# Kernel tuning notes

Measured on AMD Instinct MI355X. Metric: run time of the kernel, lower is better.

The kernel has to match this reference:

```python
import jax, jax.numpy as jnp
import numpy as np

B, S, D, H = 2, 2048, 1024, 16
HD = D // H


def setup_inputs() -> dict:
    key = jax.random.key(0)
    ks = jax.random.split(key, 6)
    scale = D ** -0.5
    return {
        "x": jax.random.normal(ks[0], (B, S, D), dtype=jnp.float32),
        "attn_mask": jnp.ones((B, S), dtype=bool),
        "wq": jax.random.normal(ks[1], (D, D), dtype=jnp.float32) * scale,
        "wk": jax.random.normal(ks[2], (D, D), dtype=jnp.float32) * scale,
        "wv": jax.random.normal(ks[3], (D, D), dtype=jnp.float32) * scale,
        "wo": jax.random.normal(ks[4], (D, D), dtype=jnp.float32) * scale,
        "bo": jax.random.normal(ks[5], (D,), dtype=jnp.float32) * 0.01,
    }


def reference(x, attn_mask, wq, wk, wv, wo, bo):
    b, s, d = x.shape
    # torch Linear: y = x @ W.T
    q = (x @ wq.T).reshape(b, s, H, HD).transpose(0, 2, 1, 3)  # (b,h,s,hd)
    k = (x @ wk.T).reshape(b, s, H, HD).transpose(0, 2, 1, 3)
    v = (x @ wv.T).reshape(b, s, H, HD).transpose(0, 2, 1, 3)
    scores = jnp.einsum("bhqd,bhkd->bhqk", q, k) * (HD ** -0.5)
    causal = jnp.triu(jnp.ones((s, s), dtype=bool), k=1)  # True above diagonal
    mask = causal[None, None, :, :] | (~attn_mask)[:, None, None, :]
    mask_value = jnp.finfo(scores.dtype).min / 2
    scores = jnp.where(mask, mask_value, scores)
    att = jax.nn.softmax(scores, axis=-1)
    ctx = jnp.einsum("bhqk,bhkd->bhqd", att, v)
    ctx = ctx.transpose(0, 2, 1, 3).reshape(b, s, d)
    return ctx @ wo.T + bo
```

## Files before the change

kernel.cpp:

```cpp
#include <hip/hip_runtime.h>
#include <stdint.h>

#define SEQ   2048
#define DMODEL 1024
#define NHEAD 16
#define HDIM  64
#define MTOT  4096

typedef short s16x8 __attribute__((ext_vector_type(8)));
typedef float f32x4 __attribute__((ext_vector_type(4)));
typedef float f32x16 __attribute__((ext_vector_type(16)));
typedef unsigned u32x4 __attribute__((ext_vector_type(4)));

#define LOG2E 1.44269504088896340736f

#if __has_builtin(__builtin_amdgcn_exp2f)
#define EXP2(x) __builtin_amdgcn_exp2f(x)
#else
#define EXP2(x) exp2f(x)
#endif

__device__ __forceinline__ short f2bf(float f) {
  union { float f; unsigned u; } v; v.f = f;
  unsigned u = v.u + 0x7fff + ((v.u >> 16) & 1);
  return (short)(u >> 16);
}

__device__ __forceinline__ void async_cp16(const void* g, void* l) {
  __builtin_amdgcn_global_load_lds(
      (const __attribute__((address_space(1))) void*)g,
      (__attribute__((address_space(3))) void*)l, 16, 0, 0);
}

__device__ __forceinline__ f32x4 mfma16(s16x8 a, s16x8 b, f32x4 c) {
  return __builtin_amdgcn_mfma_f32_16x16x32_bf16(a, b, c, 0, 0, 0);
}
__device__ __forceinline__ f32x16 mfma32(s16x8 a, s16x8 b, f32x16 c) {
  return __builtin_amdgcn_mfma_f32_32x32x16_bf16(a, b, c, 0, 0, 0);
}

__global__ __launch_bounds__(256) void cast_kernel(
    const float* __restrict__ x,  const float* __restrict__ wq,
    const float* __restrict__ wk, const float* __restrict__ wv,
    const float* __restrict__ wo,
    short* __restrict__ xb,  short* __restrict__ wqb,
    short* __restrict__ wkb, short* __restrict__ wvb, short* __restrict__ wob) {
  int i = blockIdx.x * 256 + threadIdx.x;
  const float4* src; short* dst; int off;
  const int XN = 1 << 20, WN = 1 << 18;
  if (i < XN)            { src = (const float4*)x;  dst = xb;  off = i; }
  else if (i < XN + WN)  { src = (const float4*)wq; dst = wqb; off = i - XN; }
  else if (i < XN + 2*WN){ src = (const float4*)wk; dst = wkb; off = i - XN - WN; }
  else if (i < XN + 3*WN){ src = (const float4*)wv; dst = wvb; off = i - XN - 2*WN; }
  else                   { src = (const float4*)wo; dst = wob; off = i - XN - 3*WN; }
  float4 v = src[off];
  short4 o; o.x = f2bf(v.x); o.y = f2bf(v.y); o.z = f2bf(v.z); o.w = f2bf(v.w);
  *(short4*)(dst + off * 4) = o;
}

__global__ __launch_bounds__(512, 2) void qkv_gemm(
    const short* __restrict__ xb,  const short* __restrict__ wqb,
    const short* __restrict__ wkb, const short* __restrict__ wvb,
    short* __restrict__ Q, short* __restrict__ K, short* __restrict__ Vt) {
  __shared__ short SMEM[32768];
  short (*Abuf)[4096] = reinterpret_cast<short (*)[4096]>(SMEM);
  short (*Bbuf)[3][4096] = reinterpret_cast<short (*)[3][4096]>(SMEM + 8192);
  const int tid = threadIdx.x;
  const int w = tid >> 6, lane = tid & 63;
  const int c = lane & 15, g = lane >> 4;
  const int wm = w >> 2, wn = w & 3;
  const int n0 = blockIdx.x * 128, m0 = blockIdx.y * 128;
  const int srow = lane >> 2, schunk = lane & 3;

  f32x4 acc[3][4][2] = {};

#define QKV_STAGE(KT, BS)                                                      \
  {                                                                            \
    async_cp16(xb + (m0 + w * 16 + srow) * 1024 + (KT) * 32 + schunk * 8,      \
               &Abuf[BS][w * 512]);                                            \
    async_cp16(wqb + (n0 + w * 16 + srow) * 1024 + (KT) * 32 + schunk * 8,     \
               &Bbuf[BS][0][w * 512]);                                         \
    async_cp16(wkb + (n0 + w * 16 + srow) * 1024 + (KT) * 32 + schunk * 8,     \
               &Bbuf[BS][1][w * 512]);                                         \
    async_cp16(wvb + (n0 + w * 16 + srow) * 1024 + (KT) * 32 + schunk * 8,     \
               &Bbuf[BS][2][w * 512]);                                         \
  }

  QKV_STAGE(0, 0)
  for (int kt = 0; kt < 32; ++kt) {
    __syncthreads();
    if (kt + 1 < 32) { QKV_STAGE(kt + 1, (kt + 1) & 1) }
    const int cur = kt & 1;
    s16x8 a[4];
#pragma unroll
    for (int t = 0; t < 4; ++t)
      a[t] = *(const s16x8*)&Abuf[cur][(wm * 64 + t * 16 + c) * 32 + g * 8];
#pragma unroll
    for (int z = 0; z < 3; ++z) {
      s16x8 b[2];
#pragma unroll
      for (int u = 0; u < 2; ++u)
        b[u] = *(const s16x8*)&Bbuf[cur][z][(wn * 32 + u * 16 + c) * 32 + g * 8];
#pragma unroll
      for (int t = 0; t < 4; ++t)
#pragma unroll
        for (int u = 0; u < 2; ++u)
          acc[z][t][u] = mfma16(a[t], b[u], acc[z][t][u]);
    }
  }

  short* E = SMEM;
  const int b0 = m0 >> 11, sbase = m0 & 2047, hgb = n0 >> 6;

#pragma unroll
  for (int z = 0; z < 3; ++z) {
    __syncthreads();
    if (z == 2) {
#pragma unroll
      for (int t = 0; t < 4; ++t)
#pragma unroll
        for (int u = 0; u < 2; ++u) {
          int col = wn * 32 + u * 16 + c;
          int m = wm * 64 + t * 16 + g * 4;
          int phys = (m >> 3) ^ (col & 15);
          short4 o;
          o.x = f2bf(acc[z][t][u][0]); o.y = f2bf(acc[z][t][u][1]);
          o.z = f2bf(acc[z][t][u][2]); o.w = f2bf(acc[z][t][u][3]);
          *(short4*)&E[col * 128 + phys * 8 + (m & 7)] = o;
        }
      __syncthreads();
#pragma unroll
      for (int p = 0; p < 4; ++p) {
        int R = p * 32 + (tid >> 4);
        int j = tid & 15;
        int phys = j ^ (R & 15);
        s16x8 v = *(const s16x8*)&E[R * 128 + phys * 8];
        int hloc = R >> 6, hd = R & 63;
        *(s16x8*)&Vt[(((b0 * 16 + hgb + hloc) * 64 + hd) * 2048) + sbase + j * 8] = v;
      }
    } else {
      const float scale = (z == 0) ? 0.125f * LOG2E : 1.0f;
#pragma unroll
      for (int t = 0; t < 4; ++t)
#pragma unroll
        for (int u = 0; u < 2; ++u)
#pragma unroll
          for (int r = 0; r < 4; ++r) {
            int m = wm * 64 + t * 16 + g * 4 + r;
            int col = wn * 32 + u * 16 + c;
            int phys = (col >> 3) ^ ((m >> 2) & 15);
            E[m * 128 + phys * 8 + (col & 7)] = f2bf(acc[z][t][u][r] * scale);
          }
      __syncthreads();
      short* __restrict__ dst = (z == 0) ? Q : K;
#pragma unroll
      for (int p = 0; p < 4; ++p) {
        int R = p * 64 + (tid >> 3);
        int j = tid & 7;
        int m = R >> 1, hloc = R & 1;
        int phys = (hloc * 8 + j) ^ ((m >> 2) & 15);
        s16x8 v = *(const s16x8*)&E[m * 128 + phys * 8];
        *(s16x8*)&dst[(((b0 * 16 + hgb + hloc) * 2048) + sbase + m) * 64 + j * 8] = v;
      }
    }
  }
}

#define STAGE_K(KT, BS)                                                        \
  _Pragma("unroll") for (int j = 0; j < 4; ++j) {                              \
    int idx = w * 4 + j;                                                       \
    int ks = idx >> 3, p = idx & 7;                                            \
    async_cp16(Kg + ((KT) * 128 + p * 16 + srow) * 64 + ks * 32 + sw8,         \
               &Kbuf[BS][ks][p * 512]);                                        \
  }
#define STAGE_V(KT)                                                            \
  _Pragma("unroll") for (int j = 0; j < 4; ++j) {                              \
    int idx = w * 4 + j;                                                       \
    int ks2 = idx >> 2, p = idx & 3;                                           \
    async_cp16(Vg + (p * 16 + srow) * 2048 + (KT) * 128 + ks2 * 32 + sw8,      \
               &Vlds[ks2][p * 512]);                                           \
  }

__global__ __launch_bounds__(256, 3) void attn_kernel(
    const short* __restrict__ Q, const short* __restrict__ K,
    const short* __restrict__ Vt, short* __restrict__ ctx) {
  __shared__ short Kbuf[2][2][128 * 32];
  __shared__ short Vlds[4][64 * 32];
  __shared__ float Llds[4][32];

  const int tid = threadIdx.x;
  const int w = tid >> 6, lane = tid & 63;
  const int n31 = lane & 31, h = lane >> 5;
  int bx = blockIdx.x;
  if (blockIdx.y >= 16) bx = 15 - bx;
  const int bh = blockIdx.y;
  const int qbase = bx * 128 + w * 32;
  const short* __restrict__ Qg = Q + bh * (SEQ * HDIM);
  const short* __restrict__ Kg = K + bh * (SEQ * HDIM);
  const short* __restrict__ Vg = Vt + bh * (SEQ * HDIM);
  const int srow = lane >> 2, schunk = lane & 3;
  const int sw8 = (schunk ^ ((srow >> 1) & 3)) * 8;
  const int rsw = (n31 >> 1) & 3;

  s16x8 qf[4];
#pragma unroll
  for (int ch = 0; ch < 4; ++ch)
    qf[ch] = *(const s16x8*)&Qg[(qbase + n31) * 64 + ch * 16 + h * 8];

  float l_run = 0.f;
  f32x16 oacc[2] = {};

  STAGE_K(0, 0)
  for (int kt = 0; kt <= bx; ++kt) {
    __syncthreads();
    if (kt < bx) { STAGE_K(kt + 1, (kt + 1) & 1) }
    STAGE_V(kt)

    const bool diag = (kt == bx);
    const int mtmax = diag ? w : 3;
    const short (*Kc)[128 * 32] = Kbuf[kt & 1];

    unsigned pk[4][8];
#pragma unroll
    for (int mt = 0; mt < 4; ++mt) {
      if (mt > mtmax) break;
      f32x16 st = {};
#pragma unroll
      for (int ch = 0; ch < 4; ++ch) {
        s16x8 ka = *(const s16x8*)
            &Kc[ch >> 1][(mt * 32 + n31) * 32 + ((((ch & 1) * 2 + h) ^ rsw) * 8)];
        st = mfma32(ka, qf[ch], st);
      }
      if (diag && mt == w) {
#pragma unroll
        for (int reg = 0; reg < 16; ++reg) {
          int krow = (reg & 3) + 8 * (reg >> 2) + 4 * h;
          if (krow > n31) st[reg] = -1e30f;
        }
      }
#pragma unroll
      for (int i = 0; i < 8; ++i) {
        float p0 = EXP2(st[2 * i]);
        float p1 = EXP2(st[2 * i + 1]);
        unsigned t0 = __float_as_uint(p0) & 0xffff0000u;
        unsigned t1 = __float_as_uint(p1) & 0xffff0000u;
        l_run += __uint_as_float(t0);
        l_run += __uint_as_float(t1);
        pk[mt][i] = (t0 >> 16) | t1;
      }
    }

    __syncthreads();

#pragma unroll
    for (int mt = 0; mt < 4; ++mt) {
      if (mt > mtmax) break;
#pragma unroll
      for (int kb2 = 0; kb2 < 2; ++kb2) {
        const int kb = mt * 2 + kb2;
        const unsigned q0 = pk[mt][kb2 * 4 + 0], q1 = pk[mt][kb2 * 4 + 1];
        const unsigned q2 = pk[mt][kb2 * 4 + 2], q3 = pk[mt][kb2 * 4 + 3];
        const unsigned x0 = __shfl_xor(q0, 32), x1 = __shfl_xor(q1, 32);
        const unsigned x2 = __shfl_xor(q2, 32), x3 = __shfl_xor(q3, 32);
        u32x4 av;
        av.x = h ? x2 : q0;
        av.y = h ? x3 : q1;
        av.z = h ? q2 : x0;
        av.w = h ? q3 : x1;
        s16x8 pa = __builtin_bit_cast(s16x8, av);
#pragma unroll
        for (int u = 0; u < 2; ++u) {
          s16x8 vf = *(const s16x8*)
              &Vlds[kb >> 1][(u * 32 + n31) * 32 + ((((kb & 1) * 2 + h) ^ rsw) * 8)];
          oacc[u] = mfma32(pa, vf, oacc[u]);
        }
      }
    }
  }

  float lf = l_run + __shfl_xor(l_run, 32);
  if (h == 0) Llds[w][n31] = lf;
  float inv[4][4];
#pragma unroll
  for (int gi = 0; gi < 4; ++gi) {
    float4 lv = *(const float4*)&Llds[w][gi * 8 + 4 * h];
    inv[gi][0] = 1.0f / lv.x; inv[gi][1] = 1.0f / lv.y;
    inv[gi][2] = 1.0f / lv.z; inv[gi][3] = 1.0f / lv.w;
  }

  const int b = bh >> 4, hh = bh & 15;
#pragma unroll
  for (int u = 0; u < 2; ++u)
#pragma unroll
    for (int gi = 0; gi < 4; ++gi)
#pragma unroll
      for (int ri = 0; ri < 4; ++ri) {
        int q = qbase + 8 * gi + 4 * h + ri;
        int hd = u * 32 + n31;
        ctx[(b * 2048 + q) * 1024 + hh * 64 + hd] =
            f2bf(oacc[u][gi * 4 + ri] * inv[gi][ri]);
      }
}

__global__ __launch_bounds__(256) void out_gemm(
    const short* __restrict__ ctx, const short* __restrict__ wob,
    const float* __restrict__ bo, float* __restrict__ out) {
  __shared__ short Abuf[2][128 * 32];
  __shared__ short Bbuf[2][64 * 32];
  const int tid = threadIdx.x;
  const int w = tid >> 6, lane = tid & 63;
  const int c = lane & 15, g = lane >> 4;
  const int wm = w >> 1, wn = w & 1;
  const int n0 = blockIdx.x * 64, m0 = blockIdx.y * 128;
  const int srow = lane >> 2, schunk = lane & 3;

  f32x4 acc[4][2] = {};

#define OUT_STAGE(KT, BS)                                                      \
  {                                                                            \
    _Pragma("unroll") for (int j = 0; j < 2; ++j) {                            \
      int p = w * 2 + j;                                                       \
      async_cp16(ctx + (m0 + p * 16 + srow) * 1024 + (KT) * 32 + schunk * 8,   \
                 &Abuf[BS][p * 512]);                                          \
    }                                                                          \
    async_cp16(wob + (n0 + w * 16 + srow) * 1024 + (KT) * 32 + schunk * 8,     \
               &Bbuf[BS][w * 512]);                                            \
  }

  OUT_STAGE(0, 0)
  for (int kt = 0; kt < 32; ++kt) {
    __syncthreads();
    if (kt + 1 < 32) { OUT_STAGE(kt + 1, (kt + 1) & 1) }
    const int cur = kt & 1;
    s16x8 a[4], b[2];
#pragma unroll
    for (int t = 0; t < 4; ++t)
      a[t] = *(const s16x8*)&Abuf[cur][(wm * 64 + t * 16 + c) * 32 + g * 8];
#pragma unroll
    for (int u = 0; u < 2; ++u)
      b[u] = *(const s16x8*)&Bbuf[cur][(wn * 32 + u * 16 + c) * 32 + g * 8];
#pragma unroll
    for (int t = 0; t < 4; ++t)
#pragma unroll
      for (int u = 0; u < 2; ++u)
        acc[t][u] = mfma16(a[t], b[u], acc[t][u]);
  }

#pragma unroll
  for (int t = 0; t < 4; ++t)
#pragma unroll
    for (int u = 0; u < 2; ++u) {
      int col = n0 + wn * 32 + u * 16 + c;
      float bias = bo[col];
#pragma unroll
      for (int r = 0; r < 4; ++r) {
        int m = m0 + wm * 64 + t * 16 + g * 4 + r;
        out[m * 1024 + col] = acc[t][u][r] + bias;
      }
    }
}

extern "C" void kernel_launch(void* const* d_in, const int* in_sizes, int n_in,
                              void* d_out, int out_size, void* d_ws, size_t ws_size,
                              hipStream_t stream) {
  const float* x  = (const float*)d_in[0];
  const float* wq = (const float*)d_in[2];
  const float* wk = (const float*)d_in[3];
  const float* wv = (const float*)d_in[4];
  const float* wo = (const float*)d_in[5];
  const float* bo = (const float*)d_in[6];

  char* ws = (char*)d_ws;
  short* xb  = (short*)(ws);
  short* wqb = (short*)(ws + (size_t)( 8 << 20));
  short* wkb = (short*)(ws + (size_t)(10 << 20));
  short* wvb = (short*)(ws + (size_t)(12 << 20));
  short* wob = (short*)(ws + (size_t)(14 << 20));
  short* Qb  = (short*)(ws + (size_t)(16 << 20));
  short* Kb  = (short*)(ws + (size_t)(24 << 20));
  short* Vtb = (short*)(ws + (size_t)(32 << 20));
  short* ctx = (short*)(ws + (size_t)(40 << 20));
  float* out = (float*)d_out;

  cast_kernel<<<dim3(8192), dim3(256), 0, stream>>>(x, wq, wk, wv, wo,
                                                    xb, wqb, wkb, wvb, wob);
  qkv_gemm<<<dim3(8, 32), dim3(512), 0, stream>>>(xb, wqb, wkb, wvb,
                                                  Qb, Kb, Vtb);
  attn_kernel<<<dim3(16, 32), dim3(256), 0, stream>>>(Qb, Kb, Vtb, ctx);
  out_gemm<<<dim3(16, 32), dim3(256), 0, stream>>>(ctx, wob, bo, out);
}
```

Before: 183.6 us.

## Use 32x32 MFMA with swizzled LDS in GEMMs and double attention q-tile per wave

Both projection GEMMs move from 16x16x32 to 32x32x16 bf16 MFMA and load their LDS tiles with an XOR swizzle, cutting LDS bank conflicts and the fragment loads issued per MFMA. The attention kernel now gives each wave 64 query rows (two 32-row sub-tiles) and each block 256 rows, so every K/V tile in LDS is reused by twice as many queries and the grid is halved. The cost is higher register pressure in attention (occupancy hint lowered from 3 to 2) and fewer blocks to balance the causal triangle.

Measured after the change: 232.4 us. 1.27x slower.

```diff
diff --git a/kernel.cpp b/kernel.cpp
--- a/kernel.cpp
+++ b/kernel.cpp
@@ -32,9 +32,6 @@
       (__attribute__((address_space(3))) void*)l, 16, 0, 0);
 }
 
-__device__ __forceinline__ f32x4 mfma16(s16x8 a, s16x8 b, f32x4 c) {
-  return __builtin_amdgcn_mfma_f32_16x16x32_bf16(a, b, c, 0, 0, 0);
-}
 __device__ __forceinline__ f32x16 mfma32(s16x8 a, s16x8 b, f32x16 c) {
   return __builtin_amdgcn_mfma_f32_32x32x16_bf16(a, b, c, 0, 0, 0);
 }
@@ -67,22 +64,24 @@
   short (*Bbuf)[3][4096] = reinterpret_cast<short (*)[3][4096]>(SMEM + 8192);
   const int tid = threadIdx.x;
   const int w = tid >> 6, lane = tid & 63;
-  const int c = lane & 15, g = lane >> 4;
+  const int n31 = lane & 31, hb = lane >> 5;
   const int wm = w >> 2, wn = w & 3;
   const int n0 = blockIdx.x * 128, m0 = blockIdx.y * 128;
   const int srow = lane >> 2, schunk = lane & 3;
-
-  f32x4 acc[3][4][2] = {};
+  const int sw8 = (schunk ^ ((srow >> 1) & 3)) * 8;
+  const int rsw = (n31 >> 1) & 3;
+
+  f32x16 acc[3][2] = {};
 
 #define QKV_STAGE(KT, BS)                                                      \
   {                                                                            \
-    async_cp16(xb + (m0 + w * 16 + srow) * 1024 + (KT) * 32 + schunk * 8,      \
+    async_cp16(xb + (m0 + w * 16 + srow) * 1024 + (KT) * 32 + sw8,             \
                &Abuf[BS][w * 512]);                                            \
-    async_cp16(wqb + (n0 + w * 16 + srow) * 1024 + (KT) * 32 + schunk * 8,     \
+    async_cp16(wqb + (n0 + w * 16 + srow) * 1024 + (KT) * 32 + sw8,            \
                &Bbuf[BS][0][w * 512]);                                         \
-    async_cp16(wkb + (n0 + w * 16 + srow) * 1024 + (KT) * 32 + schunk * 8,     \
+    async_cp16(wkb + (n0 + w * 16 + srow) * 1024 + (KT) * 32 + sw8,            \
                &Bbuf[BS][1][w * 512]);                                         \
-    async_cp16(wvb + (n0 + w * 16 + srow) * 1024 + (KT) * 32 + schunk * 8,     \
+    async_cp16(wvb + (n0 + w * 16 + srow) * 1024 + (KT) * 32 + sw8,            \
                &Bbuf[BS][2][w * 512]);                                         \
   }
 
@@ -91,21 +90,23 @@
     __syncthreads();
     if (kt + 1 < 32) { QKV_STAGE(kt + 1, (kt + 1) & 1) }
     const int cur = kt & 1;
-    s16x8 a[4];
-#pragma unroll
-    for (int t = 0; t < 4; ++t)
-      a[t] = *(const s16x8*)&Abuf[cur][(wm * 64 + t * 16 + c) * 32 + g * 8];
+    s16x8 a[2][2];
+#pragma unroll
+    for (int mt = 0; mt < 2; ++mt)
+#pragma unroll
+      for (int ks = 0; ks < 2; ++ks)
+        a[mt][ks] = *(const s16x8*)
+            &Abuf[cur][(wm * 64 + mt * 32 + n31) * 32 + (((ks * 2 + hb) ^ rsw) * 8)];
 #pragma unroll
     for (int z = 0; z < 3; ++z) {
-      s16x8 b[2];
-#pragma unroll
-      for (int u = 0; u < 2; ++u)
-        b[u] = *(const s16x8*)&Bbuf[cur][z][(wn * 32 + u * 16 + c) * 32 + g * 8];
-#pragma unroll
-      for (int t = 0; t < 4; ++t)
-#pragma unroll
-        for (int u = 0; u < 2; ++u)
-          acc[z][t][u] = mfma16(a[t], b[u], acc[z][t][u]);
+#pragma unroll
+      for (int ks = 0; ks < 2; ++ks) {
+        s16x8 b = *(const s16x8*)
+            &Bbuf[cur][z][(wn * 32 + n31) * 32 + (((ks * 2 + hb) ^ rsw) * 8)];
+#pragma unroll
+        for (int mt = 0; mt < 2; ++mt)
+          acc[z][mt] = mfma32(a[mt][ks], b, acc[z][mt]);
+      }
     }
   }
 
@@ -117,15 +118,15 @@
     __syncthreads();
     if (z == 2) {
 #pragma unroll
-      for (int t = 0; t < 4; ++t)
-#pragma unroll
-        for (int u = 0; u < 2; ++u) {
-          int col = wn * 32 + u * 16 + c;
-          int m = wm * 64 + t * 16 + g * 4;
+      for (int mt = 0; mt < 2; ++mt)
+#pragma unroll
+        for (int rq = 0; rq < 4; ++rq) {
+          int col = wn * 32 + n31;
+          int m = wm * 64 + mt * 32 + 8 * rq + 4 * hb;
           int phys = (m >> 3) ^ (col & 15);
           short4 o;
-          o.x = f2bf(acc[z][t][u][0]); o.y = f2bf(acc[z][t][u][1]);
-          o.z = f2bf(acc[z][t][u][2]); o.w = f2bf(acc[z][t][u][3]);
+          o.x = f2bf(acc[z][mt][rq * 4 + 0]); o.y = f2bf(acc[z][mt][rq * 4 + 1]);
+          o.z = f2bf(acc[z][mt][rq * 4 + 2]); o.w = f2bf(acc[z][mt][rq * 4 + 3]);
           *(short4*)&E[col * 128 + phys * 8 + (m & 7)] = o;
         }
       __syncthreads();
@@ -141,16 +142,14 @@
     } else {
       const float scale = (z == 0) ? 0.125f * LOG2E : 1.0f;
 #pragma unroll
-      for (int t = 0; t < 4; ++t)
-#pragma unroll
-        for (int u = 0; u < 2; ++u)
-#pragma unroll
-          for (int r = 0; r < 4; ++r) {
-            int m = wm * 64 + t * 16 + g * 4 + r;
-            int col = wn * 32 + u * 16 + c;
-            int phys = (col >> 3) ^ ((m >> 2) & 15);
-            E[m * 128 + phys * 8 + (col & 7)] = f2bf(acc[z][t][u][r] * scale);
-          }
+      for (int mt = 0; mt < 2; ++mt)
+#pragma unroll
+        for (int reg = 0; reg < 16; ++reg) {
+          int m = wm * 64 + mt * 32 + (reg & 3) + 8 * (reg >> 2) + 4 * hb;
+          int col = wn * 32 + n31;
+          int phys = (col >> 3) ^ ((m >> 2) & 15);
+          E[m * 128 + phys * 8 + (col & 7)] = f2bf(acc[z][mt][reg] * scale);
+        }
       __syncthreads();
       short* __restrict__ dst = (z == 0) ? Q : K;
 #pragma unroll
@@ -181,72 +180,82 @@
                &Vlds[ks2][p * 512]);                                           \
   }
 
-__global__ __launch_bounds__(256, 3) void attn_kernel(
+__global__ __launch_bounds__(256, 2) void attn_kernel(
     const short* __restrict__ Q, const short* __restrict__ K,
     const short* __restrict__ Vt, short* __restrict__ ctx) {
   __shared__ short Kbuf[2][2][128 * 32];
   __shared__ short Vlds[4][64 * 32];
-  __shared__ float Llds[4][32];
+  __shared__ float Llds[4][64];
 
   const int tid = threadIdx.x;
   const int w = tid >> 6, lane = tid & 63;
-  const int n31 = lane & 31, h = lane >> 5;
+  const int n31 = lane & 31, hb = lane >> 5;
   int bx = blockIdx.x;
-  if (blockIdx.y >= 16) bx = 15 - bx;
+  if (blockIdx.y >= 16) bx = 7 - bx;
   const int bh = blockIdx.y;
-  const int qbase = bx * 128 + w * 32;
+  const int qbase = bx * 256 + w * 64;
   const short* __restrict__ Qg = Q + bh * (SEQ * HDIM);
   const short* __restrict__ Kg = K + bh * (SEQ * HDIM);
   const short* __restrict__ Vg = Vt + bh * (SEQ * HDIM);
   const int srow = lane >> 2, schunk = lane & 3;
   const int sw8 = (schunk ^ ((srow >> 1) & 3)) * 8;
   const int rsw = (n31 >> 1) & 3;
-
-  s16x8 qf[4];
-#pragma unroll
-  for (int ch = 0; ch < 4; ++ch)
-    qf[ch] = *(const s16x8*)&Qg[(qbase + n31) * 64 + ch * 16 + h * 8];
-
-  float l_run = 0.f;
-  f32x16 oacc[2] = {};
+  const int qb0 = bx * 8 + w * 2;
+
+  s16x8 qf[2][4];
+#pragma unroll
+  for (int s = 0; s < 2; ++s)
+#pragma unroll
+    for (int ch = 0; ch < 4; ++ch)
+      qf[s][ch] = *(const s16x8*)
+          &Qg[(qbase + s * 32 + n31) * 64 + ch * 16 + hb * 8];
+
+  float l_run[2] = {};
+  f32x16 oacc[2][2] = {};
+  const int ktmax = 2 * bx + 1;
 
   STAGE_K(0, 0)
-  for (int kt = 0; kt <= bx; ++kt) {
+  for (int kt = 0; kt <= ktmax; ++kt) {
     __syncthreads();
-    if (kt < bx) { STAGE_K(kt + 1, (kt + 1) & 1) }
+    if (kt < ktmax) { STAGE_K(kt + 1, (kt + 1) & 1) }
     STAGE_V(kt)
 
-    const bool diag = (kt == bx);
-    const int mtmax = diag ? w : 3;
     const short (*Kc)[128 * 32] = Kbuf[kt & 1];
 
-    unsigned pk[4][8];
+    unsigned pk[2][4][8];
 #pragma unroll
     for (int mt = 0; mt < 4; ++mt) {
-      if (mt > mtmax) break;
-      f32x16 st = {};
+      const int kk = kt * 4 + mt;
+      if (kk > qb0 + 1) break;
+      f32x16 st[2] = {};
 #pragma unroll
       for (int ch = 0; ch < 4; ++ch) {
         s16x8 ka = *(const s16x8*)
-            &Kc[ch >> 1][(mt * 32 + n31) * 32 + ((((ch & 1) * 2 + h) ^ rsw) * 8)];
-        st = mfma32(ka, qf[ch], st);
-      }
-      if (diag && mt == w) {
-#pragma unroll
-        for (int reg = 0; reg < 16; ++reg) {
-          int krow = (reg & 3) + 8 * (reg >> 2) + 4 * h;
-          if (krow > n31) st[reg] = -1e30f;
+            &Kc[ch >> 1][(mt * 32 + n31) * 32 + ((((ch & 1) * 2 + hb) ^ rsw) * 8)];
+#pragma unroll
+        for (int s = 0; s < 2; ++s)
+          if (kk <= qb0 + s) st[s] = mfma32(ka, qf[s][ch], st[s]);
+      }
+#pragma unroll
+      for (int s = 0; s < 2; ++s) {
+        if (kk > qb0 + s) continue;
+        if (kk == qb0 + s) {
+#pragma unroll
+          for (int reg = 0; reg < 16; ++reg) {
+            int krow = (reg & 3) + 8 * (reg >> 2) + 4 * hb;
+            if (krow > n31) st[s][reg] = -1e30f;
+          }
         }
-      }
-#pragma unroll
-      for (int i = 0; i < 8; ++i) {
-        float p0 = EXP2(st[2 * i]);
-        float p1 = EXP2(st[2 * i + 1]);
-        unsigned t0 = __float_as_uint(p0) & 0xffff0000u;
-        unsigned t1 = __float_as_uint(p1) & 0xffff0000u;
-        l_run += __uint_as_float(t0);
-        l_run += __uint_as_float(t1);
-        pk[mt][i] = (t0 >> 16) | t1;
+#pragma unroll
+        for (int i = 0; i < 8; ++i) {
+          float p0 = EXP2(st[s][2 * i]);
+          float p1 = EXP2(st[s][2 * i + 1]);
+          unsigned t0 = __float_as_uint(p0) & 0xffff0000u;
+          unsigned t1 = __float_as_uint(p1) & 0xffff0000u;
+          l_run[s] += __uint_as_float(t0);
+          l_run[s] += __uint_as_float(t1);
+          pk[s][mt][i] = (t0 >> 16) | t1;
+        }
       }
     }
 
@@ -254,52 +263,61 @@
 
 #pragma unroll
     for (int mt = 0; mt < 4; ++mt) {
-      if (mt > mtmax) break;
+      const int kk = kt * 4 + mt;
+      if (kk > qb0 + 1) break;
 #pragma unroll
       for (int kb2 = 0; kb2 < 2; ++kb2) {
         const int kb = mt * 2 + kb2;
-        const unsigned q0 = pk[mt][kb2 * 4 + 0], q1 = pk[mt][kb2 * 4 + 1];
-        const unsigned q2 = pk[mt][kb2 * 4 + 2], q3 = pk[mt][kb2 * 4 + 3];
-        const unsigned x0 = __shfl_xor(q0, 32), x1 = __shfl_xor(q1, 32);
-        const unsigned x2 = __shfl_xor(q2, 32), x3 = __shfl_xor(q3, 32);
-        u32x4 av;
-        av.x = h ? x2 : q0;
-        av.y = h ? x3 : q1;
-        av.z = h ? q2 : x0;
-        av.w = h ? q3 : x1;
-        s16x8 pa = __builtin_bit_cast(s16x8, av);
-#pragma unroll
-        for (int u = 0; u < 2; ++u) {
-          s16x8 vf = *(const s16x8*)
-              &Vlds[kb >> 1][(u * 32 + n31) * 32 + ((((kb & 1) * 2 + h) ^ rsw) * 8)];
-          oacc[u] = mfma32(pa, vf, oacc[u]);
+        s16x8 vf[2];
+#pragma unroll
+        for (int u = 0; u < 2; ++u)
+          vf[u] = *(const s16x8*)
+              &Vlds[kb >> 1][(u * 32 + n31) * 32 + ((((kb & 1) * 2 + hb) ^ rsw) * 8)];
+#pragma unroll
+        for (int s = 0; s < 2; ++s) {
+          if (kk > qb0 + s) continue;
+          const unsigned q0 = pk[s][mt][kb2 * 4 + 0], q1 = pk[s][mt][kb2 * 4 + 1];
+          const unsigned q2 = pk[s][mt][kb2 * 4 + 2], q3 = pk[s][mt][kb2 * 4 + 3];
+          const unsigned x0 = __shfl_xor(q0, 32), x1 = __shfl_xor(q1, 32);
+          const unsigned x2 = __shfl_xor(q2, 32), x3 = __shfl_xor(q3, 32);
+          u32x4 av;
+          av.x = hb ? x2 : q0;
+          av.y = hb ? x3 : q1;
+          av.z = hb ? q2 : x0;
+          av.w = hb ? q3 : x1;
+          s16x8 pa = __builtin_bit_cast(s16x8, av);
+#pragma unroll
+          for (int u = 0; u < 2; ++u)
+            oacc[s][u] = mfma32(pa, vf[u], oacc[s][u]);
         }
       }
     }
   }
 
-  float lf = l_run + __shfl_xor(l_run, 32);
-  if (h == 0) Llds[w][n31] = lf;
-  float inv[4][4];
-#pragma unroll
-  for (int gi = 0; gi < 4; ++gi) {
-    float4 lv = *(const float4*)&Llds[w][gi * 8 + 4 * h];
-    inv[gi][0] = 1.0f / lv.x; inv[gi][1] = 1.0f / lv.y;
-    inv[gi][2] = 1.0f / lv.z; inv[gi][3] = 1.0f / lv.w;
-  }
-
+#pragma unroll
+  for (int s = 0; s < 2; ++s) {
+    float lf = l_run[s] + __shfl_xor(l_run[s], 32);
+    if (hb == 0) Llds[w][s * 32 + n31] = lf;
+  }
   const int b = bh >> 4, hh = bh & 15;
 #pragma unroll
-  for (int u = 0; u < 2; ++u)
-#pragma unroll
-    for (int gi = 0; gi < 4; ++gi)
-#pragma unroll
-      for (int ri = 0; ri < 4; ++ri) {
-        int q = qbase + 8 * gi + 4 * h + ri;
+  for (int s = 0; s < 2; ++s)
+#pragma unroll
+    for (int gi = 0; gi < 4; ++gi) {
+      float4 lv = *(const float4*)&Llds[w][s * 32 + gi * 8 + 4 * hb];
+      float inv0 = 1.0f / lv.x, inv1 = 1.0f / lv.y;
+      float inv2 = 1.0f / lv.z, inv3 = 1.0f / lv.w;
+#pragma unroll
+      for (int u = 0; u < 2; ++u) {
+        int q = qbase + s * 32 + 8 * gi + 4 * hb;
         int hd = u * 32 + n31;
-        ctx[(b * 2048 + q) * 1024 + hh * 64 + hd] =
-            f2bf(oacc[u][gi * 4 + ri] * inv[gi][ri]);
-      }
+        short* dst = &ctx[(b * 2048 + q) * 1024 + hh * 64 + hd];
+        dst[0]    = f2bf(oacc[s][u][gi * 4 + 0] * inv0);
+        dst[1024] = f2bf(oacc[s][u][gi * 4 + 1] * inv1);
+        dst[2048] = f2bf(oacc[s][u][gi * 4 + 2] * inv2);
+        dst[3072] = f2bf(oacc[s][u][gi * 4 + 3] * inv3);
+      }
+    }
 }
 
 __global__ __launch_bounds__(256) void out_gemm(
@@ -309,21 +327,23 @@
   __shared__ short Bbuf[2][64 * 32];
   const int tid = threadIdx.x;
   const int w = tid >> 6, lane = tid & 63;
-  const int c = lane & 15, g = lane >> 4;
+  const int n31 = lane & 31, hb = lane >> 5;
   const int wm = w >> 1, wn = w & 1;
   const int n0 = blockIdx.x * 64, m0 = blockIdx.y * 128;
   const int srow = lane >> 2, schunk = lane & 3;
-
-  f32x4 acc[4][2] = {};
+  const int sw8 = (schunk ^ ((srow >> 1) & 3)) * 8;
+  const int rsw = (n31 >> 1) & 3;
+
+  f32x16 acc[2] = {};
 
 #define OUT_STAGE(KT, BS)                                                      \
   {                                                                            \
     _Pragma("unroll") for (int j = 0; j < 2; ++j) {                            \
       int p = w * 2 + j;                                                       \
-      async_cp16(ctx + (m0 + p * 16 + srow) * 1024 + (KT) * 32 + schunk * 8,   \
+      async_cp16(ctx + (m0 + p * 16 + srow) * 1024 + (KT) * 32 + sw8,          \
                  &Abuf[BS][p * 512]);                                          \
     }                                                                          \
-    async_cp16(wob + (n0 + w * 16 + srow) * 1024 + (KT) * 32 + schunk * 8,     \
+    async_cp16(wob + (n0 + w * 16 + srow) * 1024 + (KT) * 32 + sw8,            \
                &Bbuf[BS][w * 512]);                                            \
   }
 
@@ -332,31 +352,27 @@
     __syncthreads();
     if (kt + 1 < 32) { OUT_STAGE(kt + 1, (kt + 1) & 1) }
     const int cur = kt & 1;
-    s16x8 a[4], b[2];
-#pragma unroll
-    for (int t = 0; t < 4; ++t)
-      a[t] = *(const s16x8*)&Abuf[cur][(wm * 64 + t * 16 + c) * 32 + g * 8];
-#pragma unroll
-    for (int u = 0; u < 2; ++u)
-      b[u] = *(const s16x8*)&Bbuf[cur][(wn * 32 + u * 16 + c) * 32 + g * 8];
-#pragma unroll
-    for (int t = 0; t < 4; ++t)
-#pragma unroll
-      for (int u = 0; u < 2; ++u)
-        acc[t][u] = mfma16(a[t], b[u], acc[t][u]);
-  }
-
-#pragma unroll
-  for (int t = 0; t < 4; ++t)
-#pragma unroll
-    for (int u = 0; u < 2; ++u) {
-      int col = n0 + wn * 32 + u * 16 + c;
-      float bias = bo[col];
-#pragma unroll
-      for (int r = 0; r < 4; ++r) {
-        int m = m0 + wm * 64 + t * 16 + g * 4 + r;
-        out[m * 1024 + col] = acc[t][u][r] + bias;
-      }
+#pragma unroll
+    for (int ks = 0; ks < 2; ++ks) {
+      s16x8 b = *(const s16x8*)
+          &Bbuf[cur][(wn * 32 + n31) * 32 + (((ks * 2 + hb) ^ rsw) * 8)];
+#pragma unroll
+      for (int mt = 0; mt < 2; ++mt) {
+        s16x8 a = *(const s16x8*)
+            &Abuf[cur][(wm * 64 + mt * 32 + n31) * 32 + (((ks * 2 + hb) ^ rsw) * 8)];
+        acc[mt] = mfma32(a, b, acc[mt]);
+      }
+    }
+  }
+
+  const int col = n0 + wn * 32 + n31;
+  const float bias = bo[col];
+#pragma unroll
+  for (int mt = 0; mt < 2; ++mt)
+#pragma unroll
+    for (int reg = 0; reg < 16; ++reg) {
+      int m = m0 + wm * 64 + mt * 32 + (reg & 3) + 8 * (reg >> 2) + 4 * hb;
+      out[m * 1024 + col] = acc[mt][reg] + bias;
     }
 }
 
@@ -386,6 +402,6 @@
                                                     xb, wqb, wkb, wvb, wob);
   qkv_gemm<<<dim3(8, 32), dim3(512), 0, stream>>>(xb, wqb, wkb, wvb,
                                                   Qb, Kb, Vtb);
-  attn_kernel<<<dim3(16, 32), dim3(256), 0, stream>>>(Qb, Kb, Vtb, ctx);
+  attn_kernel<<<dim3(8, 32), dim3(256), 0, stream>>>(Qb, Kb, Vtb, ctx);
   out_gemm<<<dim3(16, 32), dim3(256), 0, stream>>>(ctx, wob, bo, out);
 }
```
